# Performance work log

Hardware: AMD Instinct MI355X
Metric: run time of the kernel (lower is better)

Reference implementation:

```python
import jax, jax.numpy as jnp
import numpy as np

B, F, D = 4096, 64, 256  # batch, feature fields, embedding dim


def setup_inputs() -> dict:
    key = jax.random.key(0)
    inputs = jax.random.normal(key, (B, F, D), dtype=jnp.float32)
    return {"inputs": inputs}


def reference(inputs) -> jnp.ndarray:
    # Batched Gram matrix over the field axis: [B, F, F]
    gram = jnp.einsum('bid,bjd->bij', inputs, inputs)
    # Strict upper triangle (i < j), matching matrix_band_part(0,-1) - band_part(0,0)
    f = inputs.shape[1]
    iu, ju = jnp.triu_indices(f, k=1)
    # Gather the F*(F-1)/2 pairwise interactions per batch row -> [B, P]
    return gram[:, iu, ju]
```

## Files before the change

kernel.cpp:

```cpp
#include <hip/hip_runtime.h>

#define FF 64
#define DD 256
#define KC 128
#define LSTR 136
#define NPAIR 2016
#define ROWS 4
#define NCHUNK (2 * ROWS)

typedef __attribute__((ext_vector_type(8))) short short8;
typedef __attribute__((ext_vector_type(16))) float f32x16;

__device__ __forceinline__ unsigned int pack2(float lo, float hi) {
    unsigned int a = __float_as_uint(lo);
    unsigned int b = __float_as_uint(hi);
    a += 0x7FFFu + ((a >> 16) & 1u);
    b += 0x7FFFu + ((b >> 16) & 1u);
    return (a >> 16) | (b & 0xFFFF0000u);
}

__global__ __launch_bounds__(256, 4) void gram_tri(const float* __restrict__ x,
                                                   float* __restrict__ out) {
    __shared__ __align__(16) unsigned short sbuf[2][FF * LSTR];
    const int t = threadIdx.x;
    const int wave = t >> 6;
    const int lane = t & 63;
    const int b0 = blockIdx.x * ROWS;

    const int qi = wave >> 1, qj = wave & 1;
    const unsigned short* ldsA0 = &sbuf[0][(qi * 32 + (lane & 31)) * LSTR + ((lane >> 5) << 3)];
    const unsigned short* ldsB0 = &sbuf[0][(qj * 32 + (lane & 31)) * LSTR + ((lane >> 5) << 3)];
    const int bufoff = FF * LSTR;

    float4 sr[8];
    f32x16 acc;

    {
        const float4* __restrict__ src = (const float4*)(x + (size_t)b0 * (FF * DD));
#pragma unroll
        for (int it = 0; it < 8; ++it) {
            int lin = (it << 8) + t;
            sr[it] = src[((lin >> 5) << 6) + (lin & 31)];
        }
#pragma unroll
        for (int it = 0; it < 8; ++it) {
            int lin = (it << 8) + t;
            int f = lin >> 5, kq = lin & 31;
            uint2 w;
            w.x = pack2(sr[it].x, sr[it].y);
            w.y = pack2(sr[it].z, sr[it].w);
            *(uint2*)&sbuf[0][f * LSTR + (kq << 2)] = w;
        }
    }
    __syncthreads();

#pragma unroll
    for (int s = 0; s < NCHUNK; ++s) {
        if (s + 1 < NCHUNK) {
            int nb = b0 + ((s + 1) >> 1);
            int kc = ((s + 1) & 1) * KC;
            const float4* __restrict__ src = (const float4*)(x + (size_t)nb * (FF * DD) + kc);
#pragma unroll
            for (int it = 0; it < 8; ++it) {
                int lin = (it << 8) + t;
                sr[it] = src[((lin >> 5) << 6) + (lin & 31)];
            }
        }
        if ((s & 1) == 0) {
#pragma unroll
            for (int i = 0; i < 16; ++i) acc[i] = 0.0f;
        }
        if (wave != 2) {
            const unsigned short* pA = ldsA0 + (s & 1) * bufoff;
            const unsigned short* pB = ldsB0 + (s & 1) * bufoff;
#pragma unroll
            for (int ko = 0; ko < KC; ko += 16) {
                short8 a  = *(const short8*)(pA + ko);
                short8 bb = *(const short8*)(pB + ko);
                acc = __builtin_amdgcn_mfma_f32_32x32x16_bf16(a, bb, acc, 0, 0, 0);
            }
        }
        if (s + 1 < NCHUNK) {
            unsigned short* dst = &sbuf[0][((s + 1) & 1) * bufoff];
#pragma unroll
            for (int it = 0; it < 8; ++it) {
                int lin = (it << 8) + t;
                int f = lin >> 5, kq = lin & 31;
                uint2 w;
                w.x = pack2(sr[it].x, sr[it].y);
                w.y = pack2(sr[it].z, sr[it].w);
                *(uint2*)&dst[f * LSTR + (kq << 2)] = w;
            }
        }
        __syncthreads();
        if ((s & 1) && wave != 2) {
            int b = b0 + (s >> 1);
            float* __restrict__ ob = out + (size_t)b * NPAIR;
#pragma unroll
            for (int reg = 0; reg < 16; ++reg) {
                int i = (qi << 5) + (reg & 3) + ((reg >> 2) << 3) + ((lane >> 5) << 2);
                int j = (qj << 5) + (lane & 31);
                if (i < j) ob[i * 63 - ((i * (i - 1)) >> 1) + (j - i - 1)] = acc[reg];
            }
        }
    }
}

extern "C" void kernel_launch(void* const* d_in, const int* in_sizes, int n_in,
                              void* d_out, int out_size, void* d_ws, size_t ws_size,
                              hipStream_t stream) {
    const float* x = (const float*)d_in[0];
    float* out = (float*)d_out;
    gram_tri<<<4096 / ROWS, 256, 0, stream>>>(x, out);
}
```

Baseline: 361.2 us.

## Compute each batch Gram in one wave directly from registers, dropping LDS

Each wave now owns one batch row and loads fp32 inputs straight from global memory into MFMA operand fragments, converting to bf16 in registers. It computes only the three needed 32x32 quadrant blocks (skipping the redundant lower-left one) with register prefetch of the next k-slice. This removes LDS staging, block-wide barriers, and the idle-wave arrangement of the earlier version. The cost is less coalesced global loads (32-byte segments per lane) and higher register pressure, with occupancy bounds lowered to 3.

```diff
diff --git a/kernel.cpp b/kernel.cpp
--- a/kernel.cpp
+++ b/kernel.cpp
@@ -2,11 +2,7 @@
 
 #define FF 64
 #define DD 256
-#define KC 128
-#define LSTR 136
 #define NPAIR 2016
-#define ROWS 4
-#define NCHUNK (2 * ROWS)
 
 typedef __attribute__((ext_vector_type(8))) short short8;
 typedef __attribute__((ext_vector_type(16))) float f32x16;
@@ -19,90 +15,66 @@
     return (a >> 16) | (b & 0xFFFF0000u);
 }
 
-__global__ __launch_bounds__(256, 4) void gram_tri(const float* __restrict__ x,
+__device__ __forceinline__ short8 mkfrag(float4 a, float4 b) {
+    union { unsigned int u[4]; short8 s; } c;
+    c.u[0] = pack2(a.x, a.y);
+    c.u[1] = pack2(a.z, a.w);
+    c.u[2] = pack2(b.x, b.y);
+    c.u[3] = pack2(b.z, b.w);
+    return c.s;
+}
+
+__global__ __launch_bounds__(256, 3) void gram_tri(const float* __restrict__ x,
                                                    float* __restrict__ out) {
-    __shared__ __align__(16) unsigned short sbuf[2][FF * LSTR];
     const int t = threadIdx.x;
     const int wave = t >> 6;
     const int lane = t & 63;
-    const int b0 = blockIdx.x * ROWS;
+    const int b = blockIdx.x * 4 + wave;
 
-    const int qi = wave >> 1, qj = wave & 1;
-    const unsigned short* ldsA0 = &sbuf[0][(qi * 32 + (lane & 31)) * LSTR + ((lane >> 5) << 3)];
-    const unsigned short* ldsB0 = &sbuf[0][(qj * 32 + (lane & 31)) * LSTR + ((lane >> 5) << 3)];
-    const int bufoff = FF * LSTR;
+    const float4* __restrict__ src = (const float4*)(x + (size_t)b * (FF * DD));
+    const int klo = (lane >> 5) << 1;
+    const float4* __restrict__ p0 = src + (lane & 31) * (DD / 4) + klo;
+    const float4* __restrict__ p1 = p0 + 32 * (DD / 4);
 
-    float4 sr[8];
-    f32x16 acc;
+    f32x16 a00, a01, a11;
+#pragma unroll
+    for (int i = 0; i < 16; ++i) { a00[i] = 0.0f; a01[i] = 0.0f; a11[i] = 0.0f; }
 
-    {
-        const float4* __restrict__ src = (const float4*)(x + (size_t)b0 * (FF * DD));
-#pragma unroll
-        for (int it = 0; it < 8; ++it) {
-            int lin = (it << 8) + t;
-            sr[it] = src[((lin >> 5) << 6) + (lin & 31)];
-        }
-#pragma unroll
-        for (int it = 0; it < 8; ++it) {
-            int lin = (it << 8) + t;
-            int f = lin >> 5, kq = lin & 31;
-            uint2 w;
-            w.x = pack2(sr[it].x, sr[it].y);
-            w.y = pack2(sr[it].z, sr[it].w);
-            *(uint2*)&sbuf[0][f * LSTR + (kq << 2)] = w;
-        }
-    }
-    __syncthreads();
+    float4 s0a, s0b, s0c, s0d, s1a, s1b, s1c, s1d;
+    s0a = p0[0]; s0b = p0[1]; s0c = p0[4]; s0d = p0[5];
+    s1a = p1[0]; s1b = p1[1]; s1c = p1[4]; s1d = p1[5];
 
 #pragma unroll
-    for (int s = 0; s < NCHUNK; ++s) {
-        if (s + 1 < NCHUNK) {
-            int nb = b0 + ((s + 1) >> 1);
-            int kc = ((s + 1) & 1) * KC;
-            const float4* __restrict__ src = (const float4*)(x + (size_t)nb * (FF * DD) + kc);
+    for (int r = 0; r < 8; ++r) {
+        short8 f0k0 = mkfrag(s0a, s0b);
+        short8 f0k1 = mkfrag(s0c, s0d);
+        short8 f1k0 = mkfrag(s1a, s1b);
+        short8 f1k1 = mkfrag(s1c, s1d);
+        if (r < 7) {
+            const float4* __restrict__ q0 = p0 + (r + 1) * 8;
+            const float4* __restrict__ q1 = p1 + (r + 1) * 8;
+            s0a = q0[0]; s0b = q0[1]; s0c = q0[4]; s0d = q0[5];
+            s1a = q1[0]; s1b = q1[1]; s1c = q1[4]; s1d = q1[5];
+        }
+        a00 = __builtin_amdgcn_mfma_f32_32x32x16_bf16(f0k0, f0k0, a00, 0, 0, 0);
+        a01 = __builtin_amdgcn_mfma_f32_32x32x16_bf16(f0k0, f1k0, a01, 0, 0, 0);
+        a11 = __builtin_amdgcn_mfma_f32_32x32x16_bf16(f1k0, f1k0, a11, 0, 0, 0);
+        a00 = __builtin_amdgcn_mfma_f32_32x32x16_bf16(f0k1, f0k1, a00, 0, 0, 0);
+        a01 = __builtin_amdgcn_mfma_f32_32x32x16_bf16(f0k1, f1k1, a01, 0, 0, 0);
+        a11 = __builtin_amdgcn_mfma_f32_32x32x16_bf16(f1k1, f1k1, a11, 0, 0, 0);
+    }
+
+    float* __restrict__ ob = out + (size_t)b * NPAIR;
+    const int jc = lane & 31;
+    const int rbase = (lane >> 5) << 2;
 #pragma unroll
-            for (int it = 0; it < 8; ++it) {
-                int lin = (it << 8) + t;
-                sr[it] = src[((lin >> 5) << 6) + (lin & 31)];
-            }
-        }
-        if ((s & 1) == 0) {
-#pragma unroll
-            for (int i = 0; i < 16; ++i) acc[i] = 0.0f;
-        }
-        if (wave != 2) {
-            const unsigned short* pA = ldsA0 + (s & 1) * bufoff;
-            const unsigned short* pB = ldsB0 + (s & 1) * bufoff;
-#pragma unroll
-            for (int ko = 0; ko < KC; ko += 16) {
-                short8 a  = *(const short8*)(pA + ko);
-                short8 bb = *(const short8*)(pB + ko);
-                acc = __builtin_amdgcn_mfma_f32_32x32x16_bf16(a, bb, acc, 0, 0, 0);
-            }
-        }
-        if (s + 1 < NCHUNK) {
-            unsigned short* dst = &sbuf[0][((s + 1) & 1) * bufoff];
-#pragma unroll
-            for (int it = 0; it < 8; ++it) {
-                int lin = (it << 8) + t;
-                int f = lin >> 5, kq = lin & 31;
-                uint2 w;
-                w.x = pack2(sr[it].x, sr[it].y);
-                w.y = pack2(sr[it].z, sr[it].w);
-                *(uint2*)&dst[f * LSTR + (kq << 2)] = w;
-            }
-        }
-        __syncthreads();
-        if ((s & 1) && wave != 2) {
-            int b = b0 + (s >> 1);
-            float* __restrict__ ob = out + (size_t)b * NPAIR;
-#pragma unroll
-            for (int reg = 0; reg < 16; ++reg) {
-                int i = (qi << 5) + (reg & 3) + ((reg >> 2) << 3) + ((lane >> 5) << 2);
-                int j = (qj << 5) + (lane & 31);
-                if (i < j) ob[i * 63 - ((i * (i - 1)) >> 1) + (j - i - 1)] = acc[reg];
-            }
-        }
+    for (int reg = 0; reg < 16; ++reg) {
+        const int ii = (reg & 3) + ((reg >> 2) << 3) + rbase;
+        if (ii < jc) ob[ii * 63 - ((ii * (ii - 1)) >> 1) + (jc - ii - 1)] = a00[reg];
+        const int j1 = 32 + jc;
+        ob[ii * 63 - ((ii * (ii - 1)) >> 1) + (j1 - ii - 1)] = a01[reg];
+        const int i2 = 32 + ii;
+        if (i2 < j1) ob[i2 * 63 - ((i2 * (i2 - 1)) >> 1) + (j1 - i2 - 1)] = a11[reg];
     }
 }
 
@@ -111,5 +83,5 @@
                               hipStream_t stream) {
     const float* x = (const float*)d_in[0];
     float* out = (float*)d_out;
-    gram_tri<<<4096 / ROWS, 256, 0, stream>>>(x, out);
+    gram_tri<<<4096 / 4, 256, 0, stream>>>(x, out);
 }
```

Measured after the change: 371.8 us. +3.0%, slower.
